# Kernel optimization log

Hardware: AMD Instinct MI355X
Metric: run time of the kernel (lower is better)

## Reference

```python
import jax, jax.numpy as jnp
import numpy as np


def setup_inputs() -> dict:
    key = jax.random.key(0)
    k1, k2, k3 = jax.random.split(key, 3)
    B, C, N, K, O = 8, 64, 4096, 16, 64
    x = jax.random.normal(k1, (B, C, N, 1), dtype=jnp.float32)
    # 1x1 Conv2d weights (out, in*2), biases (out)
    W_edge = jax.random.normal(k2, (O, 2 * C), dtype=jnp.float32) * 0.05
    b_edge = jnp.zeros((O,), dtype=jnp.float32)
    W_att = jax.random.normal(k3, (O, 2 * C), dtype=jnp.float32) * 0.05
    b_att = jnp.zeros((O,), dtype=jnp.float32)
    return {"x": x, "W_edge": W_edge, "b_edge": b_edge,
            "W_att": W_att, "b_att": b_att, "k": K}


def reference(x, W_edge, b_edge, W_att, b_att, k):
    # x: (B, C, N, 1)
    xt = jnp.transpose(x[..., 0], (0, 2, 1))  # (B, N, C)

    # --- dense KNN via pairwise squared distance (no-grad in original) ---
    xd = jax.lax.stop_gradient(xt)
    sq = jnp.sum(xd * xd, axis=-1, keepdims=True)           # (B, N, 1)
    dist = sq - 2.0 * jnp.einsum('bnc,bmc->bnm', xd, xd) + jnp.transpose(sq, (0, 2, 1))
    _, nn_idx = jax.lax.top_k(-dist, k)                      # (B, N, k)

    # --- gather neighbor features ---
    x_j = jax.vmap(lambda feat, idx: feat[idx])(xt, nn_idx)  # (B, N, k, C)
    # center index gather is identity: x_i[b,n,kk] = xt[b,n]
    x_i = jnp.broadcast_to(xt[:, :, None, :], x_j.shape)     # (B, N, k, C)

    feat = jnp.concatenate([x_i, x_j - x_i], axis=-1)        # (B, N, k, 2C)

    # 1x1 convs == per-point linear over channels
    edge = jnp.einsum('bnkc,oc->bnko', feat, W_edge) + b_edge  # (B, N, k, O)
    attn = jnp.einsum('bnkc,oc->bnko', feat, W_att) + b_att
    attn = jax.nn.softmax(attn, axis=2)                        # softmax over k

    out = jnp.sum(edge * attn, axis=2)                         # (B, N, O)
    # match torch output layout (B, O, N, 1)
    return jnp.transpose(out, (0, 2, 1))[..., None]
```

## Files before the change

### kernel.cpp

```cpp
#include <hip/hip_runtime.h>
#include <hip/hip_bf16.h>
#include <stdint.h>

#define NB 8
#define NC 64
#define NN 4096
#define NK 16
#define NO 64
#define TILE 64
#define NCHUNK 2
#define CHCOLS (NN / NCHUNK)
#define NTILES (CHCOLS / TILE)
#define NKL 16
#define NKC 32

typedef __attribute__((ext_vector_type(8))) short bf16x8;
typedef __attribute__((ext_vector_type(4))) float f32x4;

__device__ __forceinline__ unsigned umin32(unsigned a, unsigned b) { return a < b ? a : b; }
__device__ __forceinline__ unsigned shflx(unsigned v, int m) {
  return (unsigned)__shfl_xor((int)v, m);
}
__device__ __forceinline__ unsigned fmap(float x) {
  unsigned u = __float_as_uint(x);
  return u ^ ((unsigned)((int)u >> 31) | 0x80000000u);
}
__device__ __forceinline__ float bf2f(unsigned short h) {
  return __bfloat162float(*reinterpret_cast<__hip_bfloat16*>(&h));
}
__device__ __forceinline__ unsigned short f2bfu(float v) {
  __hip_bfloat16 hh = __float2bfloat16(v);
  return *reinterpret_cast<unsigned short*>(&hh);
}

__global__ __launch_bounds__(256) void proj_kernel(
    const float* __restrict__ x, const float* __restrict__ We,
    const float* __restrict__ be, const float* __restrict__ Wa,
    unsigned short* __restrict__ PQb, float* __restrict__ sq,
    float* __restrict__ XT, unsigned short* __restrict__ H)
{
  __shared__ float xs[NC][TILE];
  __shared__ float wt[NC][192];
  const int bid = blockIdx.x;
  const int b   = bid >> 6;
  const int n0  = (bid & 63) * TILE;
  const int tid = threadIdx.x;

  const float4* xg4 = (const float4*)x;
  float4* xs4 = (float4*)xs;
  for (int i = tid; i < NC * TILE / 4; i += 256) {
    int c = i >> 4, p4 = i & 15;
    xs4[c * 16 + p4] = xg4[(b * NC + c) * (NN / 4) + (n0 >> 2) + p4];
  }
  for (int i = tid; i < 64 * NC; i += 256) {
    int o = i >> 6, c = i & 63;
    float w1 = We[o * 128 + c], w2 = We[o * 128 + 64 + c];
    wt[c][o]        = w1 - w2;
    wt[c][64 + o]   = w2;
    wt[c][128 + o]  = Wa[o * 128 + 64 + c];
  }
  __syncthreads();

  {
    const int p = tid & 63, cg = tid >> 6;
    union { float4 v4[4]; float f[16]; } vv;
    #pragma unroll
    for (int g = 0; g < 4; ++g) {
      vv.v4[g].x = xs[cg * 16 + g * 4 + 0][p];
      vv.v4[g].y = xs[cg * 16 + g * 4 + 1][p];
      vv.v4[g].z = xs[cg * 16 + g * 4 + 2][p];
      vv.v4[g].w = xs[cg * 16 + g * 4 + 3][p];
    }
    float4* Xp = (float4*)(XT + ((size_t)(b * NN + n0 + p) * NC + cg * 16));
    Xp[0] = vv.v4[0]; Xp[1] = vv.v4[1]; Xp[2] = vv.v4[2]; Xp[3] = vv.v4[3];
    union { unsigned short h[16]; uint4 u[2]; } hs;
    #pragma unroll
    for (int i = 0; i < 16; ++i) hs.h[i] = f2bfu(vv.f[i]);
    uint4* Hp = (uint4*)(H + ((size_t)(b * NN + n0 + p) * NC + cg * 16));
    Hp[0] = hs.u[0]; Hp[1] = hs.u[1];
  }

  if (tid >= 192) {
    int p = tid - 192;
    float s = 0.f;
    #pragma unroll
    for (int c = 0; c < NC; ++c) { float v = xs[c][p]; s = fmaf(v, v, s); }
    sq[b * NN + n0 + p] = s;
  } else {
    const int r = tid;
    float wreg[NC];
    #pragma unroll
    for (int c = 0; c < NC; ++c) wreg[c] = wt[c][r];
    const float bias = (r < 64) ? be[r] : 0.f;
    for (int p = 0; p < TILE; p += 4) {
      float a0 = bias, a1 = bias, a2 = bias, a3 = bias;
      #pragma unroll
      for (int c = 0; c < NC; ++c) {
        float4 xv = *(const float4*)&xs[c][p];
        a0 = fmaf(wreg[c], xv.x, a0);
        a1 = fmaf(wreg[c], xv.y, a1);
        a2 = fmaf(wreg[c], xv.z, a2);
        a3 = fmaf(wreg[c], xv.w, a3);
      }
      size_t base = (size_t)(b * NN + n0 + p) * 192 + r;
      PQb[base]           = f2bfu(a0);
      PQb[base + 192]     = f2bfu(a1);
      PQb[base + 2*192]   = f2bfu(a2);
      PQb[base + 3*192]   = f2bfu(a3);
    }
  }
}

__global__ __launch_bounds__(256) void knn_kernel(
    const unsigned short* __restrict__ H, const float* __restrict__ sq,
    unsigned short* __restrict__ cand)
{
  __shared__ unsigned short Hc[2][64 * 64];
  __shared__ unsigned short Hr[64 * 64];

  const int bid = blockIdx.x;
  const int b   = bid >> 7;
  const int rt  = (bid >> 1) & 63;
  const int ch  = bid & 1;
  const int r0  = rt * TILE;
  const int c0  = ch * CHCOLS;
  const int tid = threadIdx.x;
  const int w    = tid >> 6;
  const int lane = tid & 63;
  const int lm   = lane & 15;
  const int lk   = lane >> 4;

  const unsigned short* Hb = H + (size_t)b * NN * NC;
  const float* sqg = sq + (size_t)b * NN;

  const int rowS = tid >> 2, subS = tid & 3;
  const int bytS = rowS * 128 + subS * 32;
  const int swzS = (rowS & 7) << 4;

  {
    const uint4* srcR = (const uint4*)(Hb + (size_t)(r0 + rowS) * NC + subS * 16);
    *(uint4*)((char*)Hr + ((bytS)      ^ swzS)) = srcR[0];
    *(uint4*)((char*)Hr + ((bytS + 16) ^ swzS)) = srcR[1];
    const uint4* srcC = (const uint4*)(Hb + (size_t)(c0 + rowS) * NC + subS * 16);
    *(uint4*)((char*)Hc[0] + ((bytS)      ^ swzS)) = srcC[0];
    *(uint4*)((char*)Hc[0] + ((bytS + 16) ^ swzS)) = srcC[1];
  }
  __syncthreads();

  const int brow = w * 16 + lm;
  const int bswz = (brow & 7) << 4;
  const bf16x8 bf0 = *(const bf16x8*)((const char*)Hr + ((brow * 128 + lk * 16)      ^ bswz));
  const bf16x8 bf1 = *(const bf16x8*)((const char*)Hr + ((brow * 128 + lk * 16 + 64) ^ bswz));

  unsigned bv[NKL];
  #pragma unroll
  for (int t = 0; t < NKL; ++t) bv[t] = 0xFFFFFFFFu;
  unsigned rowGuard = 0xFFFFFFFFu;

  for (int t = 0; t < NTILES; ++t) {
    const int cur = t & 1;
    uint4 st0, st1;
    const bool doStage = (t + 1 < NTILES);
    if (doStage) {
      const uint4* src = (const uint4*)(Hb + (size_t)(c0 + (t + 1) * TILE + rowS) * NC + subS * 16);
      st0 = src[0]; st1 = src[1];
    }
    const int n1 = c0 + t * TILE;

    f32x4 acc[4];
    #pragma unroll
    for (int ct = 0; ct < 4; ++ct) acc[ct] = (f32x4){0.f, 0.f, 0.f, 0.f};
    #pragma unroll
    for (int ct = 0; ct < 4; ++ct) {
      const int arow = ct * 16 + lm;
      const int aswz = (arow & 7) << 4;
      bf16x8 a0 = *(const bf16x8*)((const char*)Hc[cur] + ((arow * 128 + lk * 16)      ^ aswz));
      bf16x8 a1 = *(const bf16x8*)((const char*)Hc[cur] + ((arow * 128 + lk * 16 + 64) ^ aswz));
      acc[ct] = __builtin_amdgcn_mfma_f32_16x16x32_bf16(a0, bf0, acc[ct], 0, 0, 0);
      acc[ct] = __builtin_amdgcn_mfma_f32_16x16x32_bf16(a1, bf1, acc[ct], 0, 0, 0);
    }

    float dd[16];
    #pragma unroll
    for (int ct = 0; ct < 4; ++ct) {
      const float4 s4 = *(const float4*)&sqg[n1 + ct * 16 + lk * 4];
      dd[ct*4+0] = fmaf(-2.f, acc[ct][0], s4.x);
      dd[ct*4+1] = fmaf(-2.f, acc[ct][1], s4.y);
      dd[ct*4+2] = fmaf(-2.f, acc[ct][2], s4.z);
      dd[ct*4+3] = fmaf(-2.f, acc[ct][3], s4.w);
    }
    float fm = dd[0];
    #pragma unroll
    for (int i = 1; i < 16; ++i) fm = fminf(fm, dd[i]);

    unsigned guard = umin32(bv[NKL - 1], rowGuard);
    const unsigned t1 = fmap(fm) & 0xFFFFF800u;
    if (__any(t1 < guard)) {
      unsigned pd[16];
      #pragma unroll
      for (int ct = 0; ct < 4; ++ct) {
        const int cbase = (t << 6) + (ct << 4) + (lk << 2);
        pd[ct*4+0] = (fmap(dd[ct*4+0]) & 0xFFFFF800u) | (unsigned)(cbase + 0);
        pd[ct*4+1] = (fmap(dd[ct*4+1]) & 0xFFFFF800u) | (unsigned)(cbase + 1);
        pd[ct*4+2] = (fmap(dd[ct*4+2]) & 0xFFFFF800u) | (unsigned)(cbase + 2);
        pd[ct*4+3] = (fmap(dd[ct*4+3]) & 0xFFFFF800u) | (unsigned)(cbase + 3);
      }
      unsigned pm = pd[0];
      #pragma unroll
      for (int i = 1; i < 16; ++i) pm = umin32(pm, pd[i]);

      #pragma unroll 1
      for (int rnd = 0; rnd < 16; ++rnd) {
        bool ins = pm < guard;
        if (!__any(ins)) break;
        unsigned x = ins ? pm : 0xFFFFFFFFu;
        const unsigned xv = x;
        #pragma unroll
        for (int i = 0; i < NKL; ++i) {
          unsigned lo = umin32(bv[i], x);
          x = bv[i] < x ? x : bv[i];
          bv[i] = lo;
        }
        #pragma unroll
        for (int i = 0; i < 16; ++i) pd[i] = (pd[i] == xv) ? 0xFFFFFFFFu : pd[i];
        pm = pd[0];
        #pragma unroll
        for (int i = 1; i < 16; ++i) pm = umin32(pm, pd[i]);
        unsigned g15 = bv[NKL - 1];
        g15 = umin32(g15, shflx(g15, 16));
        g15 = umin32(g15, shflx(g15, 32));
        rowGuard = g15;
        guard = rowGuard;
      }
    }

    if (doStage) {
      *(uint4*)((char*)Hc[cur ^ 1] + ((bytS)      ^ swzS)) = st0;
      *(uint4*)((char*)Hc[cur ^ 1] + ((bytS + 16) ^ swzS)) = st1;
    }
    __syncthreads();
  }

  unsigned* mv = (unsigned*)&Hc[0][0];
  const int myrow = w * 16 + lm;
  __syncthreads();
  #pragma unroll
  for (int t = 0; t < NKL; ++t) mv[(myrow * 4 + lk) * NKL + t] = bv[t];
  __syncthreads();
  if (lk == 0) {
    for (int s2 = 1; s2 < 4; ++s2) {
      for (int t = 0; t < NKL; ++t) {
        unsigned v = mv[(myrow * 4 + s2) * NKL + t];
        if (v >= bv[NKL - 1]) break;
        unsigned x = v;
        #pragma unroll
        for (int q = 0; q < NKL; ++q) {
          unsigned lo = umin32(bv[q], x);
          x = bv[q] < x ? x : bv[q];
          bv[q] = lo;
        }
      }
    }
    unsigned short* cp = cand + (size_t)(b * NN + r0 + myrow) * NKC + ch * NKL;
    #pragma unroll
    for (int t = 0; t < NKL; ++t)
      cp[t] = (unsigned short)((bv[t] & 0x7FFu) + c0);
  }
}

__global__ __launch_bounds__(256) void rescore_kernel(
    const float* __restrict__ XT, const float* __restrict__ sq,
    unsigned short* __restrict__ cand, int* __restrict__ nn_idx)
{
  __shared__ float dv[8][NKC];
  __shared__ unsigned short di[8][NKC];
  const int tid  = threadIdx.x;
  const int w    = tid >> 6;
  const int lane = tid & 63;
  const int rowL = w * 2 + (lane >> 5);
  const int q    = lane & 31;
  const int row  = blockIdx.x * 8 + rowL;
  const int b = row >> 12, n = row & (NN - 1);
  const float* xt  = XT + (size_t)b * NN * NC;
  const float* sqg = sq + (size_t)b * NN;

  const int j = (int)cand[(size_t)row * NKC + q];
  const float4* cj = (const float4*)(xt + (size_t)j * NC);
  const float4* cn = (const float4*)(xt + (size_t)n * NC);
  float s = 0.f;
  #pragma unroll
  for (int i = 0; i < 16; ++i) {
    float4 a = cn[i], bb = cj[i];
    s = fmaf(a.x, bb.x, s);
    s = fmaf(a.y, bb.y, s);
    s = fmaf(a.z, bb.z, s);
    s = fmaf(a.w, bb.w, s);
  }
  dv[rowL][q] = fmaf(-2.f, s, sqg[j]);
  di[rowL][q] = (unsigned short)j;
  __syncthreads();

  if (tid < 8) {
    const int row2 = blockIdx.x * 8 + tid;
    float bvv[NK]; int bbi[NK];
    #pragma unroll
    for (int p = 0; p < NK; ++p) { bvv[p] = 3.0e38f; bbi[p] = 0; }
    for (int t = 0; t < NKC; ++t) {
      float v = dv[tid][t];
      if (v < bvv[NK - 1]) {
        bvv[NK - 1] = v; bbi[NK - 1] = (int)di[tid][t];
        #pragma unroll
        for (int p = NK - 1; p > 0; --p) {
          if (bvv[p] < bvv[p - 1]) {
            float tv = bvv[p]; bvv[p] = bvv[p - 1]; bvv[p - 1] = tv;
            int   ti = bbi[p]; bbi[p] = bbi[p - 1]; bbi[p - 1] = ti;
          }
        }
      }
    }
    int* np = nn_idx + (size_t)row2 * NK;
    #pragma unroll
    for (int p = 0; p < NK; ++p) np[p] = bbi[p];
  }
}

__global__ __launch_bounds__(256) void out_kernel(
    const unsigned short* __restrict__ PQb, const int* __restrict__ nn_idx,
    float* __restrict__ out)
{
  __shared__ float ot[TILE][TILE + 1];
  const int bid = blockIdx.x;
  const int b   = bid >> 6;
  const int n0  = (bid & 63) * TILE;
  const int tid = threadIdx.x;
  const int w = tid >> 6, o = tid & 63;

  for (int pi = 0; pi < 16; ++pi) {
    const int p = w * 16 + pi;
    const int n = n0 + p;
    const unsigned short* pqn = PQb + (size_t)(b * NN + n) * 192;
    const float p1b  = bf2f(pqn[o]);
    const int* idxp  = nn_idx + (size_t)(b * NN + n) * NK;
    float p2[NK], q2[NK];
    #pragma unroll
    for (int t = 0; t < NK; ++t) {
      int jn = idxp[t];
      const unsigned short* pqj = PQb + (size_t)(b * NN + jn) * 192;
      p2[t] = bf2f(pqj[64 + o]);
      q2[t] = bf2f(pqj[128 + o]);
    }
    float m = q2[0];
    #pragma unroll
    for (int t = 1; t < NK; ++t) m = fmaxf(m, q2[t]);
    float s = 0.f, num = 0.f;
    #pragma unroll
    for (int t = 0; t < NK; ++t) {
      float e = __expf(q2[t] - m);
      s += e;
      num = fmaf(e, p1b + p2[t], num);
    }
    ot[p][o] = num / s;
  }
  __syncthreads();

  const int oo = tid >> 2, qq = tid & 3;
  float* og = out + (size_t)(b * NO + oo) * NN + n0 + qq * 16;
  #pragma unroll
  for (int i = 0; i < 4; ++i) {
    float4 v;
    v.x = ot[qq * 16 + i * 4 + 0][oo];
    v.y = ot[qq * 16 + i * 4 + 1][oo];
    v.z = ot[qq * 16 + i * 4 + 2][oo];
    v.w = ot[qq * 16 + i * 4 + 3][oo];
    *(float4*)&og[i * 4] = v;
  }
}

extern "C" void kernel_launch(void* const* d_in, const int* in_sizes, int n_in,
                              void* d_out, int out_size, void* d_ws, size_t ws_size,
                              hipStream_t stream)
{
  const float* x  = (const float*)d_in[0];
  const float* We = (const float*)d_in[1];
  const float* be = (const float*)d_in[2];
  const float* Wa = (const float*)d_in[3];
  float* out = (float*)d_out;

  char* ws = (char*)d_ws;
  size_t off = 0;
  float* sq = (float*)(ws + off);                   off += (size_t)NB * NN * 4;
  unsigned short* PQb = (unsigned short*)(ws + off); off += (size_t)NB * NN * 192 * 2;
  float* XT = (float*)(ws + off);                   off += (size_t)NB * NN * NC * 4;
  unsigned short* H = (unsigned short*)(ws + off);  off += (size_t)NB * NN * NC * 2;
  unsigned short* cand = (unsigned short*)(ws + off);
  int* nn = (int*)cand;

  dim3 blk(256);
  proj_kernel<<<dim3(NB * (NN / TILE)), blk, 0, stream>>>(x, We, be, Wa, PQb, sq, XT, H);
  knn_kernel<<<dim3(NB * (NN / TILE) * NCHUNK), blk, 0, stream>>>(H, sq, cand);
  rescore_kernel<<<dim3(NB * NN / 8), blk, 0, stream>>>(XT, sq, cand, nn);
  out_kernel<<<dim3(NB * (NN / TILE)), blk, 0, stream>>>(PQb, nn, out);
}
```

Before: 284.2 us.

## Replace per-lane register top-k in KNN with shared-memory threshold append buffer

The KNN kernel drops per-lane 16-entry sorted insertion lists and the final cross-lane merge. Each row now keeps a shared-memory candidate buffer with an atomic counter and a running distance threshold. When the buffer passes 32 entries, one lane compacts it to the best 16 and tightens the threshold. Separately, the projection kernel interleaves the P2 and Q2 columns so the output kernel fetches both neighbour values with one 32-bit load, and the row operand is loaded straight from global memory instead of through shared memory. This risks LDS atomic contention and serial single-lane compaction while other lanes wait.

```diff
diff --git a/kernel.cpp b/kernel.cpp
--- a/kernel.cpp
+++ b/kernel.cpp
@@ -11,19 +11,18 @@
 #define NCHUNK 2
 #define CHCOLS (NN / NCHUNK)
 #define NTILES (CHCOLS / TILE)
-#define NKL 16
 #define NKC 32
 
 typedef __attribute__((ext_vector_type(8))) short bf16x8;
 typedef __attribute__((ext_vector_type(4))) float f32x4;
 
-__device__ __forceinline__ unsigned umin32(unsigned a, unsigned b) { return a < b ? a : b; }
-__device__ __forceinline__ unsigned shflx(unsigned v, int m) {
-  return (unsigned)__shfl_xor((int)v, m);
-}
 __device__ __forceinline__ unsigned fmap(float x) {
   unsigned u = __float_as_uint(x);
   return u ^ ((unsigned)((int)u >> 31) | 0x80000000u);
+}
+__device__ __forceinline__ float funmap(unsigned m) {
+  unsigned u = (m & 0x80000000u) ? (m ^ 0x80000000u) : ~m;
+  return __uint_as_float(u);
 }
 __device__ __forceinline__ float bf2f(unsigned short h) {
   return __bfloat162float(*reinterpret_cast<__hip_bfloat16*>(&h));
@@ -92,6 +91,9 @@
     #pragma unroll
     for (int c = 0; c < NC; ++c) wreg[c] = wt[c][r];
     const float bias = (r < 64) ? be[r] : 0.f;
+    const int ridx = (r < 64) ? r
+                   : (r < 128) ? (64 + 2 * (r - 64))
+                               : (64 + 2 * (r - 128) + 1);
     for (int p = 0; p < TILE; p += 4) {
       float a0 = bias, a1 = bias, a2 = bias, a3 = bias;
       #pragma unroll
@@ -102,7 +104,7 @@
         a2 = fmaf(wreg[c], xv.z, a2);
         a3 = fmaf(wreg[c], xv.w, a3);
       }
-      size_t base = (size_t)(b * NN + n0 + p) * 192 + r;
+      size_t base = (size_t)(b * NN + n0 + p) * 192 + ridx;
       PQb[base]           = f2bfu(a0);
       PQb[base + 192]     = f2bfu(a1);
       PQb[base + 2*192]   = f2bfu(a2);
@@ -116,7 +118,9 @@
     unsigned short* __restrict__ cand)
 {
   __shared__ unsigned short Hc[2][64 * 64];
-  __shared__ unsigned short Hr[64 * 64];
+  __shared__ unsigned buf[64][64];
+  __shared__ int      cnt[64];
+  __shared__ float    thr[64];
 
   const int bid = blockIdx.x;
   const int b   = bid >> 7;
@@ -129,6 +133,7 @@
   const int lane = tid & 63;
   const int lm   = lane & 15;
   const int lk   = lane >> 4;
+  const int row  = w * 16 + lm;
 
   const unsigned short* Hb = H + (size_t)b * NN * NC;
   const float* sqg = sq + (size_t)b * NN;
@@ -138,24 +143,16 @@
   const int swzS = (rowS & 7) << 4;
 
   {
-    const uint4* srcR = (const uint4*)(Hb + (size_t)(r0 + rowS) * NC + subS * 16);
-    *(uint4*)((char*)Hr + ((bytS)      ^ swzS)) = srcR[0];
-    *(uint4*)((char*)Hr + ((bytS + 16) ^ swzS)) = srcR[1];
     const uint4* srcC = (const uint4*)(Hb + (size_t)(c0 + rowS) * NC + subS * 16);
     *(uint4*)((char*)Hc[0] + ((bytS)      ^ swzS)) = srcC[0];
     *(uint4*)((char*)Hc[0] + ((bytS + 16) ^ swzS)) = srcC[1];
   }
+  if (tid < 64) { cnt[tid] = 0; thr[tid] = 3.0e38f; }
+
+  const unsigned short* hrow = Hb + (size_t)(r0 + row) * NC;
+  const bf16x8 bf0 = *(const bf16x8*)(hrow + lk * 8);
+  const bf16x8 bf1 = *(const bf16x8*)(hrow + lk * 8 + 32);
   __syncthreads();
-
-  const int brow = w * 16 + lm;
-  const int bswz = (brow & 7) << 4;
-  const bf16x8 bf0 = *(const bf16x8*)((const char*)Hr + ((brow * 128 + lk * 16)      ^ bswz));
-  const bf16x8 bf1 = *(const bf16x8*)((const char*)Hr + ((brow * 128 + lk * 16 + 64) ^ bswz));
-
-  unsigned bv[NKL];
-  #pragma unroll
-  for (int t = 0; t < NKL; ++t) bv[t] = 0xFFFFFFFFu;
-  unsigned rowGuard = 0xFFFFFFFFu;
 
   for (int t = 0; t < NTILES; ++t) {
     const int cur = t & 1;
@@ -189,48 +186,82 @@
       dd[ct*4+2] = fmaf(-2.f, acc[ct][2], s4.z);
       dd[ct*4+3] = fmaf(-2.f, acc[ct][3], s4.w);
     }
-    float fm = dd[0];
-    #pragma unroll
-    for (int i = 1; i < 16; ++i) fm = fminf(fm, dd[i]);
-
-    unsigned guard = umin32(bv[NKL - 1], rowGuard);
-    const unsigned t1 = fmap(fm) & 0xFFFFF800u;
-    if (__any(t1 < guard)) {
-      unsigned pd[16];
-      #pragma unroll
-      for (int ct = 0; ct < 4; ++ct) {
-        const int cbase = (t << 6) + (ct << 4) + (lk << 2);
-        pd[ct*4+0] = (fmap(dd[ct*4+0]) & 0xFFFFF800u) | (unsigned)(cbase + 0);
-        pd[ct*4+1] = (fmap(dd[ct*4+1]) & 0xFFFFF800u) | (unsigned)(cbase + 1);
-        pd[ct*4+2] = (fmap(dd[ct*4+2]) & 0xFFFFF800u) | (unsigned)(cbase + 2);
-        pd[ct*4+3] = (fmap(dd[ct*4+3]) & 0xFFFFF800u) | (unsigned)(cbase + 3);
-      }
-      unsigned pm = pd[0];
-      #pragma unroll
-      for (int i = 1; i < 16; ++i) pm = umin32(pm, pd[i]);
-
-      #pragma unroll 1
-      for (int rnd = 0; rnd < 16; ++rnd) {
-        bool ins = pm < guard;
-        if (!__any(ins)) break;
-        unsigned x = ins ? pm : 0xFFFFFFFFu;
-        const unsigned xv = x;
-        #pragma unroll
-        for (int i = 0; i < NKL; ++i) {
-          unsigned lo = umin32(bv[i], x);
-          x = bv[i] < x ? x : bv[i];
-          bv[i] = lo;
+
+    float thrF;
+    if (t == 0) {
+      float mx = fmaxf(fmaxf(fmaxf(dd[0], dd[1]), fmaxf(dd[2], dd[3])),
+                       fmaxf(fmaxf(dd[4], dd[5]), fmaxf(dd[6], dd[7])));
+      mx = fmaxf(mx, fmaxf(fmaxf(fmaxf(dd[8], dd[9]), fmaxf(dd[10], dd[11])),
+                           fmaxf(fmaxf(dd[12], dd[13]), fmaxf(dd[14], dd[15]))));
+      mx = fminf(mx, __shfl_xor(mx, 16));
+      mx = fminf(mx, __shfl_xor(mx, 32));
+      thrF = funmap(fmap(mx) | 0x7FFu);
+      if (lk == 0) thr[row] = thrF;
+    } else {
+      thrF = thr[row];
+    }
+
+    #define APPEND1(i, half)                                                   \
+      if (dd[(half)*8 + (i)] <= thrF) {                                        \
+        const int cb = (t << 6) + ((((half)*8 + (i)) >> 2) << 4) + (lk << 2)   \
+                       + (((half)*8 + (i)) & 3);                               \
+        unsigned pk = (fmap(dd[(half)*8 + (i)]) & 0xFFFFF800u) | (unsigned)cb; \
+        int s = atomicAdd(&cnt[row], 1);                                       \
+        buf[row][s] = pk;                                                      \
+      }
+    APPEND1(0,0) APPEND1(1,0) APPEND1(2,0) APPEND1(3,0)
+    APPEND1(4,0) APPEND1(5,0) APPEND1(6,0) APPEND1(7,0)
+
+    {
+      int c = cnt[row];
+      if (c > 32 && lk == 0) {
+        unsigned sel[16];
+        #pragma unroll
+        for (int q = 0; q < 16; ++q) sel[q] = 0xFFFFFFFFu;
+        #pragma unroll 1
+        for (int k = 0; k < c; ++k) {
+          unsigned v = buf[row][k];
+          if (v < sel[15]) {
+            sel[15] = v;
+            #pragma unroll
+            for (int q = 15; q > 0; --q) {
+              if (sel[q] < sel[q-1]) { unsigned tt = sel[q]; sel[q] = sel[q-1]; sel[q-1] = tt; }
+            }
+          }
         }
         #pragma unroll
-        for (int i = 0; i < 16; ++i) pd[i] = (pd[i] == xv) ? 0xFFFFFFFFu : pd[i];
-        pm = pd[0];
-        #pragma unroll
-        for (int i = 1; i < 16; ++i) pm = umin32(pm, pd[i]);
-        unsigned g15 = bv[NKL - 1];
-        g15 = umin32(g15, shflx(g15, 16));
-        g15 = umin32(g15, shflx(g15, 32));
-        rowGuard = g15;
-        guard = rowGuard;
+        for (int q = 0; q < 16; ++q) buf[row][q] = sel[q];
+        cnt[row] = 16;
+        thr[row] = funmap(sel[15] | 0x7FFu);
+      }
+    }
+    thrF = thr[row];
+
+    APPEND1(0,1) APPEND1(1,1) APPEND1(2,1) APPEND1(3,1)
+    APPEND1(4,1) APPEND1(5,1) APPEND1(6,1) APPEND1(7,1)
+    #undef APPEND1
+
+    {
+      int c = cnt[row];
+      if (c > 32 && lk == 0) {
+        unsigned sel[16];
+        #pragma unroll
+        for (int q = 0; q < 16; ++q) sel[q] = 0xFFFFFFFFu;
+        #pragma unroll 1
+        for (int k = 0; k < c; ++k) {
+          unsigned v = buf[row][k];
+          if (v < sel[15]) {
+            sel[15] = v;
+            #pragma unroll
+            for (int q = 15; q > 0; --q) {
+              if (sel[q] < sel[q-1]) { unsigned tt = sel[q]; sel[q] = sel[q-1]; sel[q-1] = tt; }
+            }
+          }
+        }
+        #pragma unroll
+        for (int q = 0; q < 16; ++q) buf[row][q] = sel[q];
+        cnt[row] = 16;
+        thr[row] = funmap(sel[15] | 0x7FFu);
       }
     }
 
@@ -241,30 +272,26 @@
     __syncthreads();
   }
 
-  unsigned* mv = (unsigned*)&Hc[0][0];
-  const int myrow = w * 16 + lm;
-  __syncthreads();
-  #pragma unroll
-  for (int t = 0; t < NKL; ++t) mv[(myrow * 4 + lk) * NKL + t] = bv[t];
-  __syncthreads();
   if (lk == 0) {
-    for (int s2 = 1; s2 < 4; ++s2) {
-      for (int t = 0; t < NKL; ++t) {
-        unsigned v = mv[(myrow * 4 + s2) * NKL + t];
-        if (v >= bv[NKL - 1]) break;
-        unsigned x = v;
-        #pragma unroll
-        for (int q = 0; q < NKL; ++q) {
-          unsigned lo = umin32(bv[q], x);
-          x = bv[q] < x ? x : bv[q];
-          bv[q] = lo;
+    int c = cnt[row];
+    unsigned sel[16];
+    #pragma unroll
+    for (int q = 0; q < 16; ++q) sel[q] = 0xFFFFFFFFu;
+    #pragma unroll 1
+    for (int k = 0; k < c; ++k) {
+      unsigned v = buf[row][k];
+      if (v < sel[15]) {
+        sel[15] = v;
+        #pragma unroll
+        for (int q = 15; q > 0; --q) {
+          if (sel[q] < sel[q-1]) { unsigned tt = sel[q]; sel[q] = sel[q-1]; sel[q-1] = tt; }
         }
       }
     }
-    unsigned short* cp = cand + (size_t)(b * NN + r0 + myrow) * NKC + ch * NKL;
-    #pragma unroll
-    for (int t = 0; t < NKL; ++t)
-      cp[t] = (unsigned short)((bv[t] & 0x7FFu) + c0);
+    unsigned short* cp = cand + (size_t)(b * NN + r0 + row) * NKC + ch * 16;
+    #pragma unroll
+    for (int q = 0; q < 16; ++q)
+      cp[q] = (unsigned short)((sel[q] & 0x7FFu) + c0);
   }
 }
 
@@ -345,9 +372,9 @@
     #pragma unroll
     for (int t = 0; t < NK; ++t) {
       int jn = idxp[t];
-      const unsigned short* pqj = PQb + (size_t)(b * NN + jn) * 192;
-      p2[t] = bf2f(pqj[64 + o]);
-      q2[t] = bf2f(pqj[128 + o]);
+      unsigned u = *(const unsigned*)(PQb + (size_t)(b * NN + jn) * 192 + 64 + 2 * o);
+      p2[t] = bf2f((unsigned short)(u & 0xFFFFu));
+      q2[t] = bf2f((unsigned short)(u >> 16));
     }
     float m = q2[0];
     #pragma unroll
@@ -388,10 +415,10 @@
 
   char* ws = (char*)d_ws;
   size_t off = 0;
-  float* sq = (float*)(ws + off);                   off += (size_t)NB * NN * 4;
+  float* sq = (float*)(ws + off);                    off += (size_t)NB * NN * 4;
   unsigned short* PQb = (unsigned short*)(ws + off); off += (size_t)NB * NN * 192 * 2;
-  float* XT = (float*)(ws + off);                   off += (size_t)NB * NN * NC * 4;
-  unsigned short* H = (unsigned short*)(ws + off);  off += (size_t)NB * NN * NC * 2;
+  float* XT = (float*)(ws + off);                    off += (size_t)NB * NN * NC * 4;
+  unsigned short* H = (unsigned short*)(ws + off);   off += (size_t)NB * NN * NC * 2;
   unsigned short* cand = (unsigned short*)(ws + off);
   int* nn = (int*)cand;
 
```

After: 1.088 ms. +282.8%, slower.
